# Performance work log

Measured on AMD Instinct MI355X. Metric: run time of the kernel, lower is better.

Reference implementation:

```python
import jax, jax.numpy as jnp
import numpy as np
import math

B, S, D, H = 2, 2048, 2048, 16
HD = D // H  # 128


def setup_inputs() -> dict:
    key = jax.random.key(0)
    ks = jax.random.split(key, 6)
    x = jax.random.normal(ks[0], (B, S, D), dtype=jnp.float32)
    scale = 1.0 / math.sqrt(D)
    wq = jax.random.normal(ks[1], (D, D), dtype=jnp.float32) * scale
    wk = jax.random.normal(ks[2], (D, D), dtype=jnp.float32) * scale
    wv = jax.random.normal(ks[3], (D, D), dtype=jnp.float32) * scale
    wo = jax.random.normal(ks[4], (D, D), dtype=jnp.float32) * scale
    # rotary frequencies: freqs_cis[t, j] = exp(i * t / theta^(2j/HD))
    theta = 10000.0
    inv = 1.0 / (theta ** (jnp.arange(0, HD, 2, dtype=jnp.float32) / HD))  # [HD//2]
    ang = jnp.arange(S, dtype=jnp.float32)[:, None] * inv[None, :]  # [S, HD//2]
    freqs_cos = jnp.cos(ang)
    freqs_sin = jnp.sin(ang)
    # causal additive mask
    mask = jnp.where(jnp.tril(jnp.ones((S, S), dtype=bool)), 0.0, -1e9)
    mask = mask[None, None, :, :].astype(jnp.float32)
    return {"x": x, "wq": wq, "wk": wk, "wv": wv, "wo": wo,
            "freqs_cos": freqs_cos, "freqs_sin": freqs_sin, "mask": mask}


def _rope(t, cos, sin):
    # t: [B, S, H, HD]; cos/sin: [S, HD//2]
    b, s, h, d = t.shape
    t2 = t.reshape(b, s, h, d // 2, 2)
    re, im = t2[..., 0], t2[..., 1]
    c = cos[None, :, None, :]
    sn = sin[None, :, None, :]
    out_re = re * c - im * sn
    out_im = re * sn + im * c
    return jnp.stack([out_re, out_im], axis=-1).reshape(b, s, h, d)


def reference(x, wq, wk, wv, wo, freqs_cos, freqs_sin, mask):
    b, s, _ = x.shape
    xq = (x @ wq.T).reshape(b, s, H, HD)
    xk = (x @ wk.T).reshape(b, s, H, HD)
    xv = (x @ wv.T).reshape(b, s, H, HD)
    xq = _rope(xq, freqs_cos, freqs_sin)
    xk = _rope(xk, freqs_cos, freqs_sin)
    # [B, H, S, HD]
    q = xq.transpose(0, 2, 1, 3)
    k = xk.transpose(0, 2, 1, 3)
    v = xv.transpose(0, 2, 1, 3)
    scores = jnp.einsum("bhqd,bhkd->bhqk", q, k) / math.sqrt(HD)
    scores = scores + mask
    probs = jax.nn.softmax(scores.astype(jnp.float32), axis=-1).astype(q.dtype)
    out = jnp.einsum("bhqk,bhkd->bhqd", probs, v)
    out = out.transpose(0, 2, 1, 3).reshape(b, s, -1)
    return out @ wo.T
```

## Files before the change

### kernel.cpp

```cpp
#include <hip/hip_runtime.h>
#include <math.h>

#define BATCH 2
#define SEQ 2048
#define DMODEL 2048
#define NH 16
#define HD 128

typedef __bf16 bf16x8 __attribute__((ext_vector_type(8)));
typedef __bf16 bf16x4 __attribute__((ext_vector_type(4)));
typedef float f32x4 __attribute__((ext_vector_type(4)));

#define GLL16(dst, src)                                                          \
  __builtin_amdgcn_global_load_lds(                                              \
      (const __attribute__((address_space(1))) void*)(src),                      \
      (__attribute__((address_space(3))) void*)(dst), 16, 0, 0)

__global__ __launch_bounds__(256) void split_fp32(const float* __restrict__ src,
                                                  __bf16* __restrict__ hi,
                                                  __bf16* __restrict__ lo) {
  const size_t i = (size_t)blockIdx.x * 256 + threadIdx.x;
  const float4 v = ((const float4*)src)[i];
  bf16x4 h, L;
  h[0] = (__bf16)v.x; h[1] = (__bf16)v.y; h[2] = (__bf16)v.z; h[3] = (__bf16)v.w;
  L[0] = (__bf16)(v.x - (float)h[0]);
  L[1] = (__bf16)(v.y - (float)h[1]);
  L[2] = (__bf16)(v.z - (float)h[2]);
  L[3] = (__bf16)(v.w - (float)h[3]);
  ((bf16x4*)hi)[i] = h;
  ((bf16x4*)lo)[i] = L;
}

template <int EMIT>
__global__ __launch_bounds__(256) void gemm_bs(const __bf16* __restrict__ Ah,
                                               const __bf16* __restrict__ Al,
                                               const __bf16* __restrict__ Bh,
                                               const __bf16* __restrict__ Bl,
                                               void* __restrict__ Cout,
                                               int M, int N, int K) {
  __shared__ __bf16 sAh[4096], sAl[4096], sBh[4096], sBl[4096];
  const int tid = threadIdx.x;
  const int l = tid & 63;
  const int w = tid >> 6;
  const int lg = l >> 4, lm = l & 15;
  const int wr = w >> 1, wc = w & 1;
  const int m0 = blockIdx.y * 128, n0 = blockIdx.x * 128;

  const int sr = l >> 2;
  const int sc8 = (l & 3) * 8;
  const size_t rowA0 = (size_t)(m0 + 32 * w + sr);
  const size_t rowB0 = (size_t)(n0 + 32 * w + sr);

  f32x4 acc[4][4];
#pragma unroll
  for (int i = 0; i < 4; ++i)
#pragma unroll
    for (int j = 0; j < 4; ++j) { f32x4 z = {0.f, 0.f, 0.f, 0.f}; acc[i][j] = z; }

  for (int k0 = 0; k0 < K; k0 += 32) {
    __syncthreads();
    GLL16(sAh + 1024 * w,       Ah + rowA0 * K + k0 + sc8);
    GLL16(sAh + 1024 * w + 512, Ah + (rowA0 + 16) * K + k0 + sc8);
    GLL16(sAl + 1024 * w,       Al + rowA0 * K + k0 + sc8);
    GLL16(sAl + 1024 * w + 512, Al + (rowA0 + 16) * K + k0 + sc8);
    GLL16(sBh + 1024 * w,       Bh + rowB0 * K + k0 + sc8);
    GLL16(sBh + 1024 * w + 512, Bh + (rowB0 + 16) * K + k0 + sc8);
    GLL16(sBl + 1024 * w,       Bl + rowB0 * K + k0 + sc8);
    GLL16(sBl + 1024 * w + 512, Bl + (rowB0 + 16) * K + k0 + sc8);
    __syncthreads();

    bf16x8 fah[4], fal[4], fbh[4], fbl[4];
#pragma unroll
    for (int i = 0; i < 4; ++i) {
      const int ra = (wr * 64 + 16 * i + lm) * 32 + lg * 8;
      fah[i] = *(const bf16x8*)(sAh + ra);
      fal[i] = *(const bf16x8*)(sAl + ra);
      const int rb = (wc * 64 + 16 * i + lm) * 32 + lg * 8;
      fbh[i] = *(const bf16x8*)(sBh + rb);
      fbl[i] = *(const bf16x8*)(sBl + rb);
    }
#pragma unroll
    for (int i = 0; i < 4; ++i)
#pragma unroll
      for (int j = 0; j < 4; ++j) {
        acc[i][j] = __builtin_amdgcn_mfma_f32_16x16x32_bf16(fah[i], fbh[j], acc[i][j], 0, 0, 0);
        acc[i][j] = __builtin_amdgcn_mfma_f32_16x16x32_bf16(fah[i], fbl[j], acc[i][j], 0, 0, 0);
        acc[i][j] = __builtin_amdgcn_mfma_f32_16x16x32_bf16(fal[i], fbh[j], acc[i][j], 0, 0, 0);
      }
  }

#pragma unroll
  for (int i = 0; i < 4; ++i)
#pragma unroll
    for (int j = 0; j < 4; ++j)
#pragma unroll
      for (int r = 0; r < 4; ++r) {
        const size_t row = (size_t)(m0 + wr * 64 + 16 * i + lg * 4 + r);
        const size_t col = (size_t)(n0 + wc * 64 + 16 * j + lm);
        if (EMIT == 0) ((float*)Cout)[row * N + col] = acc[i][j][r];
        else           ((__bf16*)Cout)[row * N + col] = (__bf16)acc[i][j][r];
      }
}

__global__ __launch_bounds__(256) void rope_bf16(__bf16* __restrict__ t,
                                                 const float* __restrict__ cosp,
                                                 const float* __restrict__ sinp,
                                                 float scale) {
  const size_t i4 = (size_t)blockIdx.x * 256 + threadIdx.x;
  const size_t e = i4 * 4;
  const int srow = (int)((e >> 11) & 2047);
  const int p = (int)(e & 127) >> 1;
  bf16x4 vv = *(bf16x4*)(t + e);
  const float c0 = cosp[srow * 64 + p],     s0 = sinp[srow * 64 + p];
  const float c1 = cosp[srow * 64 + p + 1], s1 = sinp[srow * 64 + p + 1];
  const float re0 = (float)vv[0], im0 = (float)vv[1];
  const float re1 = (float)vv[2], im1 = (float)vv[3];
  bf16x4 o;
  o[0] = (__bf16)((re0 * c0 - im0 * s0) * scale);
  o[1] = (__bf16)((re0 * s0 + im0 * c0) * scale);
  o[2] = (__bf16)((re1 * c1 - im1 * s1) * scale);
  o[3] = (__bf16)((re1 * s1 + im1 * c1) * scale);
  *(bf16x4*)(t + e) = o;
}

__global__ __launch_bounds__(256) void attn_mfma(const __bf16* __restrict__ q,
                                                 const __bf16* __restrict__ k,
                                                 const __bf16* __restrict__ v,
                                                 __bf16* __restrict__ oh,
                                                 __bf16* __restrict__ ol) {
  __shared__ __bf16 Ks[64 * 136];
  __shared__ __align__(16) char Vt[128 * 144];
  __shared__ __bf16 Ps[64 * 72];

  const int tid = threadIdx.x;
  const int l = tid & 63, w = tid >> 6;
  const int lg = l >> 4, lm = l & 15;
  const int b = blockIdx.z, h = blockIdx.y;
  const int qt = (int)gridDim.x - 1 - (int)blockIdx.x;
  const int q0 = qt * 64;
  const size_t bh = (size_t)b * SEQ * DMODEL + (size_t)h * HD;

  bf16x8 qf[4];
  {
    const __bf16* qr = q + bh + (size_t)(q0 + 16 * w + lm) * DMODEL;
#pragma unroll
    for (int c = 0; c < 4; ++c) qf[c] = *(const bf16x8*)(qr + c * 32 + lg * 8);
  }

  f32x4 accO[8];
#pragma unroll
  for (int dt = 0; dt < 8; ++dt) { f32x4 z = {0.f, 0.f, 0.f, 0.f}; accO[dt] = z; }
  float mrun[4] = {-1e30f, -1e30f, -1e30f, -1e30f};
  float lrun[4] = {0.f, 0.f, 0.f, 0.f};

  const int srT = tid >> 4;
  const int scT = tid & 15;

  for (int kt = 0; kt <= qt; ++kt) {
    const int k0 = kt * 64;
    __syncthreads();
#pragma unroll
    for (int rnd = 0; rnd < 4; ++rnd) {
      const int r = srT + 16 * rnd;
      const size_t g = bh + (size_t)(k0 + r) * DMODEL + scT * 8;
      bf16x8 kv = *(const bf16x8*)(k + g);
      *(bf16x8*)(Ks + r * 136 + scT * 8) = kv;
      bf16x8 vv = *(const bf16x8*)(v + g);
      const int sw = (scT & 7) << 4;
#pragma unroll
      for (int e = 0; e < 8; ++e) {
        const int d = scT * 8 + e;
        *(__bf16*)(Vt + d * 144 + ((2 * r) ^ sw)) = vv[e];
      }
    }
    __syncthreads();

    f32x4 sc[4];
#pragma unroll
    for (int nt = 0; nt < 4; ++nt) { f32x4 z = {0.f, 0.f, 0.f, 0.f}; sc[nt] = z; }
#pragma unroll
    for (int nt = 0; nt < 4; ++nt)
#pragma unroll
      for (int c = 0; c < 4; ++c) {
        bf16x8 kf = *(const bf16x8*)(Ks + (nt * 16 + lm) * 136 + c * 32 + lg * 8);
        sc[nt] = __builtin_amdgcn_mfma_f32_16x16x32_bf16(qf[c], kf, sc[nt], 0, 0, 0);
      }

    if (kt == qt) {
      const int qg = q0 + 16 * w + lg * 4;
#pragma unroll
      for (int nt = 0; nt < 4; ++nt) {
        const int kg = k0 + nt * 16 + lm;
#pragma unroll
        for (int r = 0; r < 4; ++r)
          if (kg > qg + r) sc[nt][r] = -1e9f;
      }
    }

    float alpha[4];
#pragma unroll
    for (int r = 0; r < 4; ++r) {
      float mx = fmaxf(fmaxf(sc[0][r], sc[1][r]), fmaxf(sc[2][r], sc[3][r]));
      mx = fmaxf(mx, __shfl_xor(mx, 1));
      mx = fmaxf(mx, __shfl_xor(mx, 2));
      mx = fmaxf(mx, __shfl_xor(mx, 4));
      mx = fmaxf(mx, __shfl_xor(mx, 8));
      const float mnew = fmaxf(mrun[r], mx);
      alpha[r] = __expf(mrun[r] - mnew);
      float rs = 0.f;
#pragma unroll
      for (int nt = 0; nt < 4; ++nt) {
        const float p = __expf(sc[nt][r] - mnew);
        sc[nt][r] = p;
        rs += p;
      }
      rs += __shfl_xor(rs, 1);
      rs += __shfl_xor(rs, 2);
      rs += __shfl_xor(rs, 4);
      rs += __shfl_xor(rs, 8);
      lrun[r] = lrun[r] * alpha[r] + rs;
      mrun[r] = mnew;
    }
#pragma unroll
    for (int dt = 0; dt < 8; ++dt)
#pragma unroll
      for (int r = 0; r < 4; ++r) accO[dt][r] *= alpha[r];

#pragma unroll
    for (int nt = 0; nt < 4; ++nt)
#pragma unroll
      for (int r = 0; r < 4; ++r)
        Ps[(16 * w + lg * 4 + r) * 72 + nt * 16 + lm] = (__bf16)sc[nt][r];

    bf16x8 pa0 = *(const bf16x8*)(Ps + (16 * w + lm) * 72 + lg * 8);
    bf16x8 pa1 = *(const bf16x8*)(Ps + (16 * w + lm) * 72 + 32 + lg * 8);
#pragma unroll
    for (int dt = 0; dt < 8; ++dt) {
      const int d = dt * 16 + lm;
      const int sw = ((d >> 3) & 7) << 4;
      bf16x8 v0 = *(const bf16x8*)(Vt + d * 144 + ((16 * lg) ^ sw));
      bf16x8 v1 = *(const bf16x8*)(Vt + d * 144 + ((64 + 16 * lg) ^ sw));
      accO[dt] = __builtin_amdgcn_mfma_f32_16x16x32_bf16(pa0, v0, accO[dt], 0, 0, 0);
      accO[dt] = __builtin_amdgcn_mfma_f32_16x16x32_bf16(pa1, v1, accO[dt], 0, 0, 0);
    }
  }

  float invl[4];
#pragma unroll
  for (int r = 0; r < 4; ++r) invl[r] = 1.f / lrun[r];
#pragma unroll
  for (int dt = 0; dt < 8; ++dt)
#pragma unroll
    for (int r = 0; r < 4; ++r) {
      const float val = accO[dt][r] * invl[r];
      const size_t oidx = bh + (size_t)(q0 + 16 * w + lg * 4 + r) * DMODEL + dt * 16 + lm;
      const __bf16 hv = (__bf16)val;
      oh[oidx] = hv;
      ol[oidx] = (__bf16)(val - (float)hv);
    }
}

extern "C" void kernel_launch(void* const* d_in, const int* in_sizes, int n_in,
                              void* d_out, int out_size, void* d_ws, size_t ws_size,
                              hipStream_t stream) {
  const float* x  = (const float*)d_in[0];
  const float* wq = (const float*)d_in[1];
  const float* wk = (const float*)d_in[2];
  const float* wv = (const float*)d_in[3];
  const float* wo = (const float*)d_in[4];
  const float* fc = (const float*)d_in[5];
  const float* fs = (const float*)d_in[6];

  const size_t NTOK = (size_t)BATCH * SEQ;
  const size_t NE   = NTOK * DMODEL;

  char* wsb = (char*)d_ws;
  __bf16* xh = (__bf16*)wsb;
  __bf16* xl = xh + NE;
  __bf16* wh = (__bf16*)(wsb + 2 * NE * 2);
  __bf16* wl = wh + (size_t)DMODEL * DMODEL;
  __bf16* vb = (__bf16*)(wsb + 2 * NE * 2 + 2 * (size_t)DMODEL * DMODEL * 2);
  __bf16* oh = xh;
  __bf16* ol = xl;
  __bf16* qb = (__bf16*)d_out;
  __bf16* kb = qb + NE;

  const dim3 gg(DMODEL / 128, (unsigned)(NTOK / 128));
  const int sx = (int)(NE / 4 / 256);
  const int sw = DMODEL * DMODEL / 4 / 256;

  split_fp32<<<sx, 256, 0, stream>>>(x, xh, xl);

  split_fp32<<<sw, 256, 0, stream>>>(wq, wh, wl);
  gemm_bs<1><<<gg, 256, 0, stream>>>(xh, xl, wh, wl, qb, (int)NTOK, DMODEL, DMODEL);
  split_fp32<<<sw, 256, 0, stream>>>(wk, wh, wl);
  gemm_bs<1><<<gg, 256, 0, stream>>>(xh, xl, wh, wl, kb, (int)NTOK, DMODEL, DMODEL);
  split_fp32<<<sw, 256, 0, stream>>>(wv, wh, wl);
  gemm_bs<1><<<gg, 256, 0, stream>>>(xh, xl, wh, wl, vb, (int)NTOK, DMODEL, DMODEL);

  rope_bf16<<<sx, 256, 0, stream>>>(qb, fc, fs, 0.08838834764831845f);
  rope_bf16<<<sx, 256, 0, stream>>>(kb, fc, fs, 1.0f);

  attn_mfma<<<dim3(SEQ / 64, NH, BATCH), 256, 0, stream>>>(qb, kb, vb, oh, ol);

  split_fp32<<<sw, 256, 0, stream>>>(wo, wh, wl);
  gemm_bs<0><<<gg, 256, 0, stream>>>(oh, ol, wh, wl, (float*)d_out, (int)NTOK, DMODEL, DMODEL);
}
```

Measured before the change: 785.2 us.

## Rewrite attention with 32x32 MFMA, 128-row query tiles and register prefetch

Replaces the flash-attention kernel with one that uses 32x32x16 bf16 MFMAs computing S^T so probabilities stay in registers: they are repacked with cross-lane shuffles instead of going through a shared-memory P buffer. Query tiles grow to 128 rows (32 per wave), K/V for the next tile are prefetched into registers during compute, the K layout in shared memory is XOR-swizzled, rescaling is skipped when no row max changes, and blocks are remapped with a flattened grid. Fully masked tiles are skipped per wave. This raises register pressure and keeps the scalar per-element V transpose stores, and attention is only one part of a pipeline dominated by GEMMs.

```diff
diff --git a/kernel.cpp b/kernel.cpp
--- a/kernel.cpp
+++ b/kernel.cpp
@@ -10,6 +10,7 @@
 typedef __bf16 bf16x8 __attribute__((ext_vector_type(8)));
 typedef __bf16 bf16x4 __attribute__((ext_vector_type(4)));
 typedef float f32x4 __attribute__((ext_vector_type(4)));
+typedef float f32x16 __attribute__((ext_vector_type(16)));
 
 #define GLL16(dst, src)                                                          \
   __builtin_amdgcn_global_load_lds(                                              \
@@ -123,141 +124,186 @@
   *(bf16x4*)(t + e) = o;
 }
 
-__global__ __launch_bounds__(256) void attn_mfma(const __bf16* __restrict__ q,
-                                                 const __bf16* __restrict__ k,
-                                                 const __bf16* __restrict__ v,
-                                                 __bf16* __restrict__ oh,
-                                                 __bf16* __restrict__ ol) {
-  __shared__ __bf16 Ks[64 * 136];
+static __device__ __forceinline__ unsigned pk2(float a, float b) {
+  unsigned short x = __builtin_bit_cast(unsigned short, (__bf16)a);
+  unsigned short y = __builtin_bit_cast(unsigned short, (__bf16)b);
+  return ((unsigned)y << 16) | (unsigned)x;
+}
+
+__global__ __launch_bounds__(256) void attn_mfma2(const __bf16* __restrict__ q,
+                                                  const __bf16* __restrict__ k,
+                                                  const __bf16* __restrict__ v,
+                                                  __bf16* __restrict__ oh,
+                                                  __bf16* __restrict__ ol) {
+  __shared__ __align__(16) char Ks[64 * 272];
   __shared__ __align__(16) char Vt[128 * 144];
-  __shared__ __bf16 Ps[64 * 72];
 
   const int tid = threadIdx.x;
   const int l = tid & 63, w = tid >> 6;
-  const int lg = l >> 4, lm = l & 15;
-  const int b = blockIdx.z, h = blockIdx.y;
-  const int qt = (int)gridDim.x - 1 - (int)blockIdx.x;
-  const int q0 = qt * 64;
+  const int l31 = l & 31, hg = l >> 5;
+
+  const int f = (int)blockIdx.x;
+  const int X = f & 7, t = f >> 3;
+  const int g = X * 4 + (t & 3);
+  const int qt = 15 - (t >> 2);
+  const int b = g >> 4, h = g & 15;
+  const int q0 = qt * 128;
   const size_t bh = (size_t)b * SEQ * DMODEL + (size_t)h * HD;
 
-  bf16x8 qf[4];
+  bf16x8 qf[8];
   {
-    const __bf16* qr = q + bh + (size_t)(q0 + 16 * w + lm) * DMODEL;
-#pragma unroll
-    for (int c = 0; c < 4; ++c) qf[c] = *(const bf16x8*)(qr + c * 32 + lg * 8);
-  }
-
-  f32x4 accO[8];
-#pragma unroll
-  for (int dt = 0; dt < 8; ++dt) { f32x4 z = {0.f, 0.f, 0.f, 0.f}; accO[dt] = z; }
-  float mrun[4] = {-1e30f, -1e30f, -1e30f, -1e30f};
-  float lrun[4] = {0.f, 0.f, 0.f, 0.f};
+    const __bf16* qr = q + bh + (size_t)(q0 + 32 * w + l31) * DMODEL;
+#pragma unroll
+    for (int ks = 0; ks < 8; ++ks) qf[ks] = *(const bf16x8*)(qr + ks * 16 + hg * 8);
+  }
+
+  f32x16 accO[4];
+#pragma unroll
+  for (int dt = 0; dt < 4; ++dt)
+#pragma unroll
+    for (int i = 0; i < 16; ++i) accO[dt][i] = 0.f;
+  float m_own = -1e30f, l_own = 0.f;
 
   const int srT = tid >> 4;
   const int scT = tid & 15;
-
-  for (int kt = 0; kt <= qt; ++kt) {
+  const int nkt = 2 * qt + 2;
+  const int qg_own = q0 + 32 * w + l31;
+  const int qg_min = q0 + 32 * w;
+
+  bf16x8 kst[4], vst[4];
+#pragma unroll
+  for (int rnd = 0; rnd < 4; ++rnd) {
+    const int r = srT + 16 * rnd;
+    const size_t ga = bh + (size_t)(r) * DMODEL + scT * 8;
+    kst[rnd] = *(const bf16x8*)(k + ga);
+    vst[rnd] = *(const bf16x8*)(v + ga);
+  }
+
+  for (int kt = 0; kt < nkt; ++kt) {
     const int k0 = kt * 64;
     __syncthreads();
 #pragma unroll
     for (int rnd = 0; rnd < 4; ++rnd) {
       const int r = srT + 16 * rnd;
-      const size_t g = bh + (size_t)(k0 + r) * DMODEL + scT * 8;
-      bf16x8 kv = *(const bf16x8*)(k + g);
-      *(bf16x8*)(Ks + r * 136 + scT * 8) = kv;
-      bf16x8 vv = *(const bf16x8*)(v + g);
-      const int sw = (scT & 7) << 4;
-#pragma unroll
-      for (int e = 0; e < 8; ++e) {
-        const int d = scT * 8 + e;
-        *(__bf16*)(Vt + d * 144 + ((2 * r) ^ sw)) = vv[e];
-      }
+      *(bf16x8*)(Ks + r * 272 + ((scT * 16) ^ (((r >> 3) & 7) << 4))) = kst[rnd];
+      const int swz = (scT & 7) << 4;
+      const int cb = (2 * r) ^ swz;
+#pragma unroll
+      for (int e = 0; e < 8; ++e)
+        *(__bf16*)(Vt + (scT * 8 + e) * 144 + cb) = vst[rnd][e];
     }
     __syncthreads();
-
-    f32x4 sc[4];
-#pragma unroll
-    for (int nt = 0; nt < 4; ++nt) { f32x4 z = {0.f, 0.f, 0.f, 0.f}; sc[nt] = z; }
-#pragma unroll
-    for (int nt = 0; nt < 4; ++nt)
-#pragma unroll
-      for (int c = 0; c < 4; ++c) {
-        bf16x8 kf = *(const bf16x8*)(Ks + (nt * 16 + lm) * 136 + c * 32 + lg * 8);
-        sc[nt] = __builtin_amdgcn_mfma_f32_16x16x32_bf16(qf[c], kf, sc[nt], 0, 0, 0);
-      }
-
-    if (kt == qt) {
-      const int qg = q0 + 16 * w + lg * 4;
-#pragma unroll
-      for (int nt = 0; nt < 4; ++nt) {
-        const int kg = k0 + nt * 16 + lm;
-#pragma unroll
-        for (int r = 0; r < 4; ++r)
-          if (kg > qg + r) sc[nt][r] = -1e9f;
-      }
-    }
-
-    float alpha[4];
-#pragma unroll
-    for (int r = 0; r < 4; ++r) {
-      float mx = fmaxf(fmaxf(sc[0][r], sc[1][r]), fmaxf(sc[2][r], sc[3][r]));
-      mx = fmaxf(mx, __shfl_xor(mx, 1));
-      mx = fmaxf(mx, __shfl_xor(mx, 2));
-      mx = fmaxf(mx, __shfl_xor(mx, 4));
-      mx = fmaxf(mx, __shfl_xor(mx, 8));
-      const float mnew = fmaxf(mrun[r], mx);
-      alpha[r] = __expf(mrun[r] - mnew);
-      float rs = 0.f;
-#pragma unroll
-      for (int nt = 0; nt < 4; ++nt) {
-        const float p = __expf(sc[nt][r] - mnew);
-        sc[nt][r] = p;
+    if (kt + 1 < nkt) {
+#pragma unroll
+      for (int rnd = 0; rnd < 4; ++rnd) {
+        const int r = srT + 16 * rnd;
+        const size_t ga = bh + (size_t)((kt + 1) * 64 + r) * DMODEL + scT * 8;
+        kst[rnd] = *(const bf16x8*)(k + ga);
+        vst[rnd] = *(const bf16x8*)(v + ga);
+      }
+    }
+    if (k0 > qg_min + 31) continue;
+
+    f32x16 sc[2];
+#pragma unroll
+    for (int mt = 0; mt < 2; ++mt)
+#pragma unroll
+      for (int i = 0; i < 16; ++i) sc[mt][i] = 0.f;
+#pragma unroll
+    for (int mt = 0; mt < 2; ++mt) {
+      const int row = mt * 32 + l31;
+      const char* kr = Ks + row * 272;
+      const int sx = ((row >> 3) & 7) << 4;
+#pragma unroll
+      for (int ks = 0; ks < 8; ++ks) {
+        bf16x8 kf = *(const bf16x8*)(kr + ((ks * 32 + hg * 16) ^ sx));
+        sc[mt] = __builtin_amdgcn_mfma_f32_32x32x16_bf16(kf, qf[ks], sc[mt], 0, 0, 0);
+      }
+    }
+
+    if (k0 + 63 > qg_min) {
+#pragma unroll
+      for (int mt = 0; mt < 2; ++mt)
+#pragma unroll
+        for (int ri = 0; ri < 16; ++ri) {
+          const int kg = k0 + mt * 32 + (ri & 3) + 8 * (ri >> 2) + 4 * hg;
+          if (kg > qg_own) sc[mt][ri] = -INFINITY;
+        }
+    }
+
+    float tm = -INFINITY;
+#pragma unroll
+    for (int mt = 0; mt < 2; ++mt)
+#pragma unroll
+      for (int ri = 0; ri < 16; ++ri) tm = fmaxf(tm, sc[mt][ri]);
+    tm = fmaxf(tm, __shfl_xor(tm, 32));
+
+    if (__any(tm > m_own)) {
+      const float mnew = fmaxf(m_own, tm);
+      const float alpha = __expf(m_own - mnew);
+      m_own = mnew;
+      l_own *= alpha;
+#pragma unroll
+      for (int ri = 0; ri < 16; ++ri) {
+        const float a = __shfl(alpha, (ri & 3) + 8 * (ri >> 2) + 4 * hg);
+#pragma unroll
+        for (int dt = 0; dt < 4; ++dt) accO[dt][ri] *= a;
+      }
+    }
+    float rs = 0.f;
+#pragma unroll
+    for (int mt = 0; mt < 2; ++mt)
+#pragma unroll
+      for (int ri = 0; ri < 16; ++ri) {
+        const float p = __expf(sc[mt][ri] - m_own);
+        sc[mt][ri] = p;
         rs += p;
       }
-      rs += __shfl_xor(rs, 1);
-      rs += __shfl_xor(rs, 2);
-      rs += __shfl_xor(rs, 4);
-      rs += __shfl_xor(rs, 8);
-      lrun[r] = lrun[r] * alpha[r] + rs;
-      mrun[r] = mnew;
-    }
-#pragma unroll
-    for (int dt = 0; dt < 8; ++dt)
-#pragma unroll
-      for (int r = 0; r < 4; ++r) accO[dt][r] *= alpha[r];
-
-#pragma unroll
-    for (int nt = 0; nt < 4; ++nt)
-#pragma unroll
-      for (int r = 0; r < 4; ++r)
-        Ps[(16 * w + lg * 4 + r) * 72 + nt * 16 + lm] = (__bf16)sc[nt][r];
-
-    bf16x8 pa0 = *(const bf16x8*)(Ps + (16 * w + lm) * 72 + lg * 8);
-    bf16x8 pa1 = *(const bf16x8*)(Ps + (16 * w + lm) * 72 + 32 + lg * 8);
-#pragma unroll
-    for (int dt = 0; dt < 8; ++dt) {
-      const int d = dt * 16 + lm;
-      const int sw = ((d >> 3) & 7) << 4;
-      bf16x8 v0 = *(const bf16x8*)(Vt + d * 144 + ((16 * lg) ^ sw));
-      bf16x8 v1 = *(const bf16x8*)(Vt + d * 144 + ((64 + 16 * lg) ^ sw));
-      accO[dt] = __builtin_amdgcn_mfma_f32_16x16x32_bf16(pa0, v0, accO[dt], 0, 0, 0);
-      accO[dt] = __builtin_amdgcn_mfma_f32_16x16x32_bf16(pa1, v1, accO[dt], 0, 0, 0);
-    }
-  }
-
-  float invl[4];
-#pragma unroll
-  for (int r = 0; r < 4; ++r) invl[r] = 1.f / lrun[r];
-#pragma unroll
-  for (int dt = 0; dt < 8; ++dt)
-#pragma unroll
-    for (int r = 0; r < 4; ++r) {
-      const float val = accO[dt][r] * invl[r];
-      const size_t oidx = bh + (size_t)(q0 + 16 * w + lg * 4 + r) * DMODEL + dt * 16 + lm;
+    rs += __shfl_xor(rs, 32);
+    l_own += rs;
+
+#pragma unroll
+    for (int kk = 0; kk < 4; ++kk) {
+      const int mt = kk >> 1, J8 = (kk & 1) * 8;
+      unsigned oL0 = pk2(sc[mt][J8 + 0], sc[mt][J8 + 1]);
+      unsigned oL1 = pk2(sc[mt][J8 + 2], sc[mt][J8 + 3]);
+      unsigned oH0 = pk2(sc[mt][J8 + 4], sc[mt][J8 + 5]);
+      unsigned oH1 = pk2(sc[mt][J8 + 6], sc[mt][J8 + 7]);
+      unsigned s0 = hg ? oL0 : oH0;
+      unsigned s1 = hg ? oL1 : oH1;
+      const unsigned r0 = (unsigned)__shfl_xor((int)s0, 32);
+      const unsigned r1 = (unsigned)__shfl_xor((int)s1, 32);
+      int4 fi;
+      fi.x = (int)(hg ? r0 : oL0);
+      fi.y = (int)(hg ? r1 : oL1);
+      fi.z = (int)(hg ? oH0 : r0);
+      fi.w = (int)(hg ? oH1 : r1);
+      const bf16x8 pa = __builtin_bit_cast(bf16x8, fi);
+      const int kb = (kk * 32 + hg * 16);
+#pragma unroll
+      for (int dt = 0; dt < 4; ++dt) {
+        const int d = dt * 32 + l31;
+        bf16x8 vf = *(const bf16x8*)(Vt + d * 144 + (kb ^ (((d >> 3) & 7) << 4)));
+        accO[dt] = __builtin_amdgcn_mfma_f32_32x32x16_bf16(pa, vf, accO[dt], 0, 0, 0);
+      }
+    }
+  }
+
+  const float inv_own = 1.f / l_own;
+#pragma unroll
+  for (int ri = 0; ri < 16; ++ri) {
+    const int row = (ri & 3) + 8 * (ri >> 2) + 4 * hg;
+    const float il = __shfl(inv_own, row & 31);
+    const size_t rbase = bh + (size_t)(q0 + 32 * w + row) * DMODEL;
+#pragma unroll
+    for (int dt = 0; dt < 4; ++dt) {
+      const float val = accO[dt][ri] * il;
+      const size_t idx = rbase + dt * 32 + l31;
       const __bf16 hv = (__bf16)val;
-      oh[oidx] = hv;
-      ol[oidx] = (__bf16)(val - (float)hv);
-    }
+      oh[idx] = hv;
+      ol[idx] = (__bf16)(val - (float)hv);
+    }
+  }
 }
 
 extern "C" void kernel_launch(void* const* d_in, const int* in_sizes, int n_in,
@@ -301,7 +347,7 @@
   rope_bf16<<<sx, 256, 0, stream>>>(qb, fc, fs, 0.08838834764831845f);
   rope_bf16<<<sx, 256, 0, stream>>>(kb, fc, fs, 1.0f);
 
-  attn_mfma<<<dim3(SEQ / 64, NH, BATCH), 256, 0, stream>>>(qb, kb, vb, oh, ol);
+  attn_mfma2<<<dim3(512), 256, 0, stream>>>(qb, kb, vb, oh, ol);
 
   split_fp32<<<sw, 256, 0, stream>>>(wo, wh, wl);
   gemm_bs<0><<<gg, 256, 0, stream>>>(oh, ol, wh, wl, (float*)d_out, (int)NTOK, DMODEL, DMODEL);
```

Result: faster. 670.0 us (-14.7%).
